# Kernel tuning notes

Hardware: AMD Instinct MI355X
Metric: run time of the kernel (lower is better)

The kernel has to match this reference:

```python
import jax, jax.numpy as jnp
import numpy as np

B, L, D_E = 2, 2048, 1024
H, D_Q = 16, 64
EPS = 1e-5


def setup_inputs() -> dict:
    key = jax.random.key(0)
    ks = jax.random.split(key, 12)
    s_in = 1.0 / np.sqrt(D_E)
    s_mid = 1.0 / np.sqrt(H * D_Q)
    return {
        "pre_q": jax.random.normal(ks[0], (B, L, D_E), jnp.float32),
        "pre_k": jax.random.normal(ks[1], (B, L, D_E), jnp.float32),
        "Wq": jax.random.normal(ks[2], (D_E, H * D_Q), jnp.float32) * s_in,
        "bq": jnp.zeros((H * D_Q,), jnp.float32),
        "Wk": jax.random.normal(ks[3], (D_E, H * D_Q), jnp.float32) * s_in,
        "bk": jnp.zeros((H * D_Q,), jnp.float32),
        "Wv": jax.random.normal(ks[4], (D_E, H * D_Q), jnp.float32) * s_in,
        "bv": jnp.zeros((H * D_Q,), jnp.float32),
        "Wo": jax.random.normal(ks[5], (H * D_Q, D_E), jnp.float32) * s_mid,
        "bo": jnp.zeros((D_E,), jnp.float32),
        "gamma": jnp.ones((D_E,), jnp.float32),
        "beta": jnp.zeros((D_E,), jnp.float32),
    }


def reference(pre_q, pre_k, Wq, bq, Wk, bk, Wv, bv, Wo, bo, gamma, beta):
    b, ql, _ = pre_q.shape
    kl = pre_k.shape[1]
    q = (pre_q @ Wq + bq).reshape(b, ql, H, D_Q)
    k = (pre_k @ Wk + bk).reshape(b, kl, H, D_Q)
    v = (pre_k @ Wv + bv).reshape(b, kl, H, D_Q)
    scores = jnp.einsum('bqhd,bkhd->bhqk', q, k) / jnp.sqrt(jnp.float32(D_Q))
    attn = jax.nn.softmax(scores, axis=-1)
    ctx = jnp.einsum('bhqk,bkhd->bqhd', attn, v).reshape(b, ql, H * D_Q)
    out = ctx @ Wo + bo
    x = pre_q + out
    mu = jnp.mean(x, axis=-1, keepdims=True)
    var = jnp.mean(jnp.square(x - mu), axis=-1, keepdims=True)
    return (x - mu) * jax.lax.rsqrt(var + EPS) * gamma + beta
```

## Files before the change

kernel.cpp:

```cpp
#include <hip/hip_runtime.h>
#include <hip/hip_bf16.h>
#include <cstdint>

typedef unsigned short ushort_t;
typedef __attribute__((ext_vector_type(8))) short short8;
typedef __attribute__((ext_vector_type(8))) __bf16 bf16x8;
typedef __attribute__((ext_vector_type(4))) float f32x4;
typedef __attribute__((ext_vector_type(4))) ushort_t ushort4v;
typedef __attribute__((ext_vector_type(2))) unsigned int uint2v;
typedef __attribute__((ext_vector_type(4))) unsigned int uint4v;

__device__ inline ushort_t f2bf(float f) {
    union { float f; unsigned u; } x; x.f = f;
    unsigned r = x.u + 0x7fffu + ((x.u >> 16) & 1u);
    return (ushort_t)(r >> 16);
}

__device__ inline unsigned pkbf(float a, float b) {
    __hip_bfloat162 h = __float22bfloat162_rn(float2{a, b});
    unsigned r;
    __builtin_memcpy(&r, &h, 4);
    return r;
}

__device__ inline unsigned pktrunc(float a, float b) {
    return __builtin_amdgcn_perm(__builtin_bit_cast(unsigned, b),
                                 __builtin_bit_cast(unsigned, a), 0x07060302u);
}

#if __has_builtin(__builtin_amdgcn_exp2f)
#define EXP2(x) __builtin_amdgcn_exp2f(x)
#else
#define EXP2(x) __builtin_exp2f(x)
#endif

__device__ inline bf16x8 ldfrag(const ushort_t* p) {
    short8 s = *(const short8*)p;
    return __builtin_bit_cast(bf16x8, s);
}

__device__ inline f32x4 mfma16(bf16x8 a, bf16x8 b, f32x4 c) {
    return __builtin_amdgcn_mfma_f32_16x16x32_bf16(a, b, c, 0, 0, 0);
}

__device__ inline void glds16(const ushort_t* g, ushort_t* l) {
    __builtin_amdgcn_global_load_lds((const __attribute__((address_space(1))) void*)g,
                                     (__attribute__((address_space(3))) void*)l, 16, 0, 0);
}

__global__ __launch_bounds__(256) void prep_k(const float* __restrict__ a, const float* __restrict__ b,
                                              ushort_t* __restrict__ oa, ushort_t* __restrict__ ob,
                                              const float* __restrict__ W0, const float* __restrict__ W1,
                                              const float* __restrict__ W2, const float* __restrict__ W3,
                                              ushort_t* __restrict__ wout) {
    const int blk = blockIdx.x;
    const int t = threadIdx.x;
    if (blk < 4096) {
        int i = (blk * 256 + t) * 4;
        float4 va = *(const float4*)(a + i);
        float4 vb = *(const float4*)(b + i);
        ushort4v pa = {f2bf(va.x), f2bf(va.y), f2bf(va.z), f2bf(va.w)};
        ushort4v pb = {f2bf(vb.x), f2bf(vb.y), f2bf(vb.z), f2bf(vb.w)};
        *(ushort4v*)(oa + i) = pa;
        *(ushort4v*)(ob + i) = pb;
    } else {
        const int rem = blk - 4096;
        const int z = rem >> 10;
        const int bx = (rem & 31) * 32, by = ((rem >> 5) & 31) * 32;
        const float* W = (z == 0) ? W0 : (z == 1) ? W1 : (z == 2) ? W2 : W3;
        ushort_t* o = wout + (size_t)z * (1u << 20);
        __shared__ float tile[32][33];
        const int tx = t & 31, ty = t >> 5;
#pragma unroll
        for (int r = 0; r < 4; ++r)
            tile[ty + r * 8][tx] = W[(size_t)(by + ty + r * 8) * 1024 + bx + tx];
        __syncthreads();
#pragma unroll
        for (int r = 0; r < 4; ++r)
            o[(size_t)(bx + ty + r * 8) * 1024 + by + tx] = f2bf(tile[tx][ty + r * 8]);
    }
}

template <int MODE>
__global__ __launch_bounds__(256) void gemm128(
    const ushort_t* __restrict__ A1, const ushort_t* __restrict__ A2,
    const ushort_t* __restrict__ Wt,
    const float* __restrict__ bias0, const float* __restrict__ bias1, const float* __restrict__ bias2,
    ushort_t* __restrict__ oQ, ushort_t* __restrict__ oK, ushort_t* __restrict__ oVt,
    const float* __restrict__ resid, float* __restrict__ oX) {
    const int t = threadIdx.x;
    const int phys = blockIdx.x;
    const int bid = (MODE == 0) ? (phys & 7) * 96 + (phys >> 3)
                                : (phys & 7) * 32 + (phys >> 3);
    int g, mb, nb;
    const float* bias;
    const ushort_t* Ab;
    const ushort_t* Wg;
    if (MODE == 0) {
        g = bid >> 8;
        const int rem = bid & 255;
        mb = rem >> 3;
        nb = rem & 7;
        Wg = Wt + (size_t)g * (1u << 20);
        bias = (g == 0) ? bias0 : (g == 1) ? bias1 : bias2;
        Ab = (g == 0) ? A1 : A2;
    } else {
        g = 0;
        mb = bid >> 3;
        nb = bid & 7;
        Wg = Wt;
        bias = bias0;
        Ab = A1;
    }
    const int m0 = mb * 128, n0 = nb * 128;

    __shared__ ushort_t As[3][128 * 32];
    __shared__ ushort_t Bs[3][128 * 32];
    const int row4 = t >> 2, c8 = (t & 3) * 8;
    const ushort_t* Ag = Ab + (size_t)(m0 + row4) * 1024 + c8;
    const ushort_t* Bg = Wg + (size_t)(n0 + row4) * 1024 + c8;
    const int ldst = row4 * 32 + c8;

    const int lane = t & 63, wid = t >> 6;
    const int wm = wid >> 1, wn = wid & 1;
    const int lr = lane & 15, lgp = lane >> 4, lk = lgp * 8;

    f32x4 acc[4][4];
#pragma unroll
    for (int j = 0; j < 4; ++j) {
        const f32x4 bj = *(const f32x4*)(bias + n0 + wn * 64 + j * 16 + 4 * lgp);
#pragma unroll
        for (int i = 0; i < 4; ++i) acc[j][i] = bj;
    }

#define STAGE(buf, kt)                                          \
    {                                                           \
        glds16(Ag + (kt), &As[buf][ldst]);                      \
        glds16(Ag + (kt) + 64 * 1024, &As[buf][ldst + 2048]);   \
        glds16(Bg + (kt), &Bs[buf][ldst]);                      \
        glds16(Bg + (kt) + 64 * 1024, &Bs[buf][ldst + 2048]);   \
    }

#define COMPUTE(buf)                                                              \
    {                                                                             \
        bf16x8 af[4], bfr[4];                                                     \
        _Pragma("unroll") for (int i = 0; i < 4; ++i)                             \
            af[i] = ldfrag(&As[buf][(wm * 64 + i * 16 + lr) * 32 + lk]);          \
        _Pragma("unroll") for (int j = 0; j < 4; ++j)                             \
            bfr[j] = ldfrag(&Bs[buf][(wn * 64 + j * 16 + lr) * 32 + lk]);         \
        __builtin_amdgcn_s_setprio(1);                                            \
        _Pragma("unroll") for (int j = 0; j < 4; ++j)                             \
            _Pragma("unroll") for (int i = 0; i < 4; ++i)                         \
                acc[j][i] = mfma16(bfr[j], af[i], acc[j][i]);                     \
        __builtin_amdgcn_s_setprio(0);                                            \
    }

#define GITER(it, buf, buf2)                                                      \
    {                                                                             \
        if ((it) <= 30) { asm volatile("s_waitcnt vmcnt(4)" ::: "memory"); }      \
        else            { asm volatile("s_waitcnt vmcnt(0)" ::: "memory"); }      \
        __syncthreads();                                                          \
        if ((it) + 2 < 32) STAGE(buf2, ((it) + 2) * 32);                          \
        COMPUTE(buf)                                                              \
    }

    STAGE(0, 0);
    STAGE(1, 32);
    for (int b3 = 0; b3 < 30; b3 += 3) {
        GITER(b3 + 0, 0, 2)
        GITER(b3 + 1, 1, 0)
        GITER(b3 + 2, 2, 1)
    }
    GITER(30, 0, 2)
    GITER(31, 1, 0)
#undef STAGE
#undef COMPUTE
#undef GITER

    const float qs = (MODE == 0 && g == 0) ? 0.18033688011f : 1.0f;

#pragma unroll
    for (int j = 0; j < 4; ++j) {
        const int n = n0 + wn * 64 + j * 16 + 4 * lgp;
#pragma unroll
        for (int i = 0; i < 4; ++i) {
            const f32x4 v = acc[j][i];
            const int m = m0 + wm * 64 + i * 16 + lr;
            if (MODE == 0) {
                const int b = m >> 11, ll = m & 2047;
                const int h = n >> 6, d = n & 63;
                if (g == 2) {
                    const int lp = (ll & ~63) | (ll & 32) | (((ll >> 2) & 3) << 3)
                                 | (((ll >> 4) & 1) << 2) | (ll & 3);
#pragma unroll
                    for (int jj = 0; jj < 4; ++jj)
                        oVt[((size_t)(b * 16 + h) * 64 + d + jj) * 2048 + lp] = f2bf(v[jj]);
                } else {
                    uint2v cw = {pkbf(v[0] * qs, v[1] * qs), pkbf(v[2] * qs, v[3] * qs)};
                    ushort_t* dst = (g == 0) ? oQ : oK;
                    *(uint2v*)(dst + (((size_t)(b * 16 + h) * 2048) + ll) * 64 + d) = cw;
                }
            } else {
                const float4 r = *(const float4*)(resid + (size_t)m * 1024 + n);
                float4 o;
                o.x = v[0] + r.x; o.y = v[1] + r.y; o.z = v[2] + r.z; o.w = v[3] + r.w;
                *(float4*)(oX + (size_t)m * 1024 + n) = o;
            }
        }
    }
}

__global__ __launch_bounds__(256, 2) void attn_k(const ushort_t* __restrict__ Qg, const ushort_t* __restrict__ Kg,
                                                 const ushort_t* __restrict__ Vtg, ushort_t* __restrict__ Cg) {
    __shared__ ushort_t Ks[2][8 * 512];
    __shared__ ushort_t Vs[2][8 * 512];

    const int t = threadIdx.x;
    const int lane = t & 63, w = t >> 6;
    const int bid = blockIdx.x;
    const int xcd = bid & 7, j = bid >> 3;
    const int bh = (xcd << 2) | (j >> 4);
    const int qb = j & 15;
    const int q0 = qb * 128 + w * 32;
    const int lr = lane & 15, g = lane >> 4;
    const int srow = lane & 15, sch = lane >> 4;

    const ushort_t* Kbase = Kg + (size_t)bh * (2048 * 64);
    const ushort_t* Vbase = Vtg + (size_t)bh * (64 * 2048);

    const ushort_t* QpA = Qg + ((size_t)bh * 2048 + q0 + lr) * 64 + g * 8;
    const bf16x8 qA0 = ldfrag(QpA), qA1 = ldfrag(QpA + 32);
    const bf16x8 qB0 = ldfrag(QpA + 16 * 64), qB1 = ldfrag(QpA + 16 * 64 + 32);

    f32x4 oA[4] = {}, oB[4] = {};
    float lA = 0.f, lB = 0.f;

#define STAGE(buf, kt)                                                                        \
    {                                                                                         \
        glds16(Kbase + (size_t)((kt) + 16 * w + srow) * 64 + sch * 8, &Ks[buf][w * 512 + lane * 8]);            \
        glds16(Kbase + (size_t)((kt) + 16 * w + srow) * 64 + 32 + sch * 8, &Ks[buf][(4 + w) * 512 + lane * 8]); \
        glds16(Vbase + (size_t)(16 * w + srow) * 2048 + (kt) + sch * 8, &Vs[buf][(2 * w) * 512 + lane * 8]);    \
        glds16(Vbase + (size_t)(16 * w + srow) * 2048 + (kt) + 32 + sch * 8, &Vs[buf][(2 * w + 1) * 512 + lane * 8]); \
    }

#define COMPUTE(BUF)                                                                      \
    {                                                                                     \
        f32x4 stA[4], stB[4];                                                             \
        _Pragma("unroll") for (int f = 0; f < 4; ++f) {                                   \
            const bf16x8 k0 = ldfrag(&Ks[BUF][f * 512 + lane * 8]);                       \
            const bf16x8 k1 = ldfrag(&Ks[BUF][(4 + f) * 512 + lane * 8]);                 \
            f32x4 sA = {}, sB = {};                                                       \
            sA = mfma16(k0, qA0, sA);                                                     \
            sA = mfma16(k1, qA1, sA);                                                     \
            sB = mfma16(k0, qB0, sB);                                                     \
            sB = mfma16(k1, qB1, sB);                                                     \
            stA[f] = sA;                                                                  \
            stB[f] = sB;                                                                  \
        }                                                                                 \
        unsigned pkA[8], pkB[8];                                                          \
        float rsA = 0.f, rsB = 0.f;                                                       \
        _Pragma("unroll") for (int f = 0; f < 4; ++f) {                                   \
            const float a0 = EXP2(stA[f][0]);                                             \
            const float a1 = EXP2(stA[f][1]);                                             \
            const float a2 = EXP2(stA[f][2]);                                             \
            const float a3 = EXP2(stA[f][3]);                                             \
            rsA += (a0 + a1) + (a2 + a3);                                                 \
            pkA[2 * f] = pktrunc(a0, a1);                                                 \
            pkA[2 * f + 1] = pktrunc(a2, a3);                                             \
            const float b0 = EXP2(stB[f][0]);                                             \
            const float b1 = EXP2(stB[f][1]);                                             \
            const float b2 = EXP2(stB[f][2]);                                             \
            const float b3 = EXP2(stB[f][3]);                                             \
            rsB += (b0 + b1) + (b2 + b3);                                                 \
            pkB[2 * f] = pktrunc(b0, b1);                                                 \
            pkB[2 * f + 1] = pktrunc(b2, b3);                                             \
        }                                                                                 \
        lA += rsA;                                                                        \
        lB += rsB;                                                                        \
        _Pragma("unroll") for (int b = 0; b < 2; ++b) {                                   \
            const uint4v ua = {pkA[4 * b], pkA[4 * b + 1], pkA[4 * b + 2], pkA[4 * b + 3]}; \
            const uint4v ub = {pkB[4 * b], pkB[4 * b + 1], pkB[4 * b + 2], pkB[4 * b + 3]}; \
            const bf16x8 pA = __builtin_bit_cast(bf16x8, ua);                             \
            const bf16x8 pB = __builtin_bit_cast(bf16x8, ub);                             \
            _Pragma("unroll") for (int df = 0; df < 4; ++df) {                            \
                const bf16x8 vf = ldfrag(&Vs[BUF][(2 * df + b) * 512 + (g * 16 + lr) * 8]); \
                oA[df] = mfma16(vf, pA, oA[df]);                                          \
                oB[df] = mfma16(vf, pB, oB[df]);                                          \
            }                                                                             \
        }                                                                                 \
    }

    STAGE(0, 0);
    asm volatile("s_waitcnt vmcnt(0)" ::: "memory");
    __syncthreads();

    for (int kt2 = 0; kt2 < 2048; kt2 += 128) {
        STAGE(1, kt2 + 64);
        COMPUTE(0)
        asm volatile("s_waitcnt vmcnt(0)" ::: "memory");
        __syncthreads();
        if (kt2 + 128 < 2048) STAGE(0, kt2 + 128);
        COMPUTE(1)
        asm volatile("s_waitcnt vmcnt(0)" ::: "memory");
        __syncthreads();
    }
#undef STAGE
#undef COMPUTE

    lA += __shfl_xor(lA, 16, 64);
    lA += __shfl_xor(lA, 32, 64);
    lB += __shfl_xor(lB, 16, 64);
    lB += __shfl_xor(lB, 32, 64);

    const int bb = bh >> 4, hh = bh & 15;
    {
        const float inv = 1.0f / lA;
        ushort_t* cp = Cg + ((size_t)(bb * 2048 + q0 + lr) * 1024) + hh * 64;
#pragma unroll
        for (int df = 0; df < 4; ++df) {
            uint2v cw = {pkbf(oA[df][0] * inv, oA[df][1] * inv), pkbf(oA[df][2] * inv, oA[df][3] * inv)};
            *(uint2v*)(cp + 16 * df + 4 * g) = cw;
        }
    }
    {
        const float inv = 1.0f / lB;
        ushort_t* cp = Cg + ((size_t)(bb * 2048 + q0 + 16 + lr) * 1024) + hh * 64;
#pragma unroll
        for (int df = 0; df < 4; ++df) {
            uint2v cw = {pkbf(oB[df][0] * inv, oB[df][1] * inv), pkbf(oB[df][2] * inv, oB[df][3] * inv)};
            *(uint2v*)(cp + 16 * df + 4 * g) = cw;
        }
    }
}

__global__ __launch_bounds__(256) void ln_k(const float* __restrict__ X, const float* __restrict__ gamma,
                                            const float* __restrict__ beta, float* __restrict__ out) {
    const int row = blockIdx.x, t = threadIdx.x;
    const float4 x = ((const float4*)(X + (size_t)row * 1024))[t];
    float s = x.x + x.y + x.z + x.w;
    float s2 = x.x * x.x + x.y * x.y + x.z * x.z + x.w * x.w;
#pragma unroll
    for (int m = 1; m < 64; m <<= 1) {
        s += __shfl_xor(s, m, 64);
        s2 += __shfl_xor(s2, m, 64);
    }
    __shared__ float rs[4], rq[4];
    if ((t & 63) == 0) { rs[t >> 6] = s; rq[t >> 6] = s2; }
    __syncthreads();
    const float S = rs[0] + rs[1] + rs[2] + rs[3];
    const float S2 = rq[0] + rq[1] + rq[2] + rq[3];
    const float mu = S * (1.0f / 1024.0f);
    const float var = S2 * (1.0f / 1024.0f) - mu * mu;
    const float r = rsqrtf(var + 1e-5f);
    const float4 gg = ((const float4*)gamma)[t];
    const float4 bb = ((const float4*)beta)[t];
    float4 o;
    o.x = (x.x - mu) * r * gg.x + bb.x;
    o.y = (x.y - mu) * r * gg.y + bb.y;
    o.z = (x.z - mu) * r * gg.z + bb.z;
    o.w = (x.w - mu) * r * gg.w + bb.w;
    ((float4*)(out + (size_t)row * 1024))[t] = o;
}

extern "C" void kernel_launch(void* const* d_in, const int* in_sizes, int n_in,
                              void* d_out, int out_size, void* d_ws, size_t ws_size,
                              hipStream_t stream) {
    (void)in_sizes; (void)n_in; (void)out_size; (void)ws_size;
    const float* pre_q = (const float*)d_in[0];
    const float* pre_k = (const float*)d_in[1];
    const float* Wq = (const float*)d_in[2];
    const float* bq = (const float*)d_in[3];
    const float* Wk = (const float*)d_in[4];
    const float* bk = (const float*)d_in[5];
    const float* Wv = (const float*)d_in[6];
    const float* bv = (const float*)d_in[7];
    const float* Wo = (const float*)d_in[8];
    const float* bo = (const float*)d_in[9];
    const float* gamma = (const float*)d_in[10];
    const float* beta = (const float*)d_in[11];
    float* out = (float*)d_out;
    char* ws = (char*)d_ws;
    const size_t MB = 1024 * 1024;
    ushort_t* Xq = (ushort_t*)(ws);
    ushort_t* Xk = (ushort_t*)(ws + 8 * MB);
    ushort_t* Wt = (ushort_t*)(ws + 16 * MB);
    ushort_t* Qb = (ushort_t*)(ws + 24 * MB);
    ushort_t* Kb = (ushort_t*)(ws + 32 * MB);
    ushort_t* Vt = (ushort_t*)(ws + 40 * MB);
    ushort_t* CTX = (ushort_t*)(ws + 48 * MB);
    float* Xres = (float*)(ws + 24 * MB);

    prep_k<<<8192, 256, 0, stream>>>(pre_q, pre_k, Xq, Xk, Wq, Wk, Wv, Wo, Wt);
    gemm128<0><<<768, 256, 0, stream>>>(Xq, Xk, Wt, bq, bk, bv, Qb, Kb, Vt, nullptr, nullptr);
    attn_k<<<512, 256, 0, stream>>>(Qb, Kb, Vt, CTX);
    gemm128<1><<<256, 256, 0, stream>>>(CTX, nullptr, Wt + 3 * (1u << 20), bo, nullptr, nullptr,
                                        nullptr, nullptr, nullptr, pre_q, Xres);
    ln_k<<<4096, 256, 0, stream>>>(Xres, gamma, beta, out);
}
```

Measured before the change: 125.6 us.

## Fuse fp32-to-bf16 activation conversion into QKV GEMM and store residual as bf16

After: 124.4 us (median of 2 runs). Within noise of the previous version (-0.9%).

```diff
diff --git a/kernel.cpp b/kernel.cpp
--- a/kernel.cpp
+++ b/kernel.cpp
@@ -23,6 +23,11 @@
     return r;
 }
 
+__device__ inline float bf2f(ushort_t u) {
+    unsigned v = (unsigned)u << 16;
+    return __builtin_bit_cast(float, v);
+}
+
 __device__ inline unsigned pktrunc(float a, float b) {
     return __builtin_amdgcn_perm(__builtin_bit_cast(unsigned, b),
                                  __builtin_bit_cast(unsigned, a), 0x07060302u);
@@ -48,53 +53,40 @@
                                      (__attribute__((address_space(3))) void*)l, 16, 0, 0);
 }
 
-__global__ __launch_bounds__(256) void prep_k(const float* __restrict__ a, const float* __restrict__ b,
-                                              ushort_t* __restrict__ oa, ushort_t* __restrict__ ob,
-                                              const float* __restrict__ W0, const float* __restrict__ W1,
+__global__ __launch_bounds__(256) void prep_k(const float* __restrict__ W0, const float* __restrict__ W1,
                                               const float* __restrict__ W2, const float* __restrict__ W3,
                                               ushort_t* __restrict__ wout) {
     const int blk = blockIdx.x;
     const int t = threadIdx.x;
-    if (blk < 4096) {
-        int i = (blk * 256 + t) * 4;
-        float4 va = *(const float4*)(a + i);
-        float4 vb = *(const float4*)(b + i);
-        ushort4v pa = {f2bf(va.x), f2bf(va.y), f2bf(va.z), f2bf(va.w)};
-        ushort4v pb = {f2bf(vb.x), f2bf(vb.y), f2bf(vb.z), f2bf(vb.w)};
-        *(ushort4v*)(oa + i) = pa;
-        *(ushort4v*)(ob + i) = pb;
-    } else {
-        const int rem = blk - 4096;
-        const int z = rem >> 10;
-        const int bx = (rem & 31) * 32, by = ((rem >> 5) & 31) * 32;
-        const float* W = (z == 0) ? W0 : (z == 1) ? W1 : (z == 2) ? W2 : W3;
-        ushort_t* o = wout + (size_t)z * (1u << 20);
-        __shared__ float tile[32][33];
-        const int tx = t & 31, ty = t >> 5;
-#pragma unroll
-        for (int r = 0; r < 4; ++r)
-            tile[ty + r * 8][tx] = W[(size_t)(by + ty + r * 8) * 1024 + bx + tx];
-        __syncthreads();
-#pragma unroll
-        for (int r = 0; r < 4; ++r)
-            o[(size_t)(bx + ty + r * 8) * 1024 + by + tx] = f2bf(tile[tx][ty + r * 8]);
-    }
+    const int z = blk >> 10;
+    const int bx = (blk & 31) * 32, by = ((blk >> 5) & 31) * 32;
+    const float* W = (z == 0) ? W0 : (z == 1) ? W1 : (z == 2) ? W2 : W3;
+    ushort_t* o = wout + (size_t)z * (1u << 20);
+    __shared__ float tile[32][33];
+    const int tx = t & 31, ty = t >> 5;
+#pragma unroll
+    for (int r = 0; r < 4; ++r)
+        tile[ty + r * 8][tx] = W[(size_t)(by + ty + r * 8) * 1024 + bx + tx];
+    __syncthreads();
+#pragma unroll
+    for (int r = 0; r < 4; ++r)
+        o[(size_t)(bx + ty + r * 8) * 1024 + by + tx] = f2bf(tile[tx][ty + r * 8]);
 }
 
 template <int MODE>
 __global__ __launch_bounds__(256) void gemm128(
-    const ushort_t* __restrict__ A1, const ushort_t* __restrict__ A2,
+    const float* __restrict__ Af1, const float* __restrict__ Af2,
+    const ushort_t* __restrict__ A1,
     const ushort_t* __restrict__ Wt,
     const float* __restrict__ bias0, const float* __restrict__ bias1, const float* __restrict__ bias2,
     ushort_t* __restrict__ oQ, ushort_t* __restrict__ oK, ushort_t* __restrict__ oVt,
-    const float* __restrict__ resid, float* __restrict__ oX) {
+    const float* __restrict__ resid, ushort_t* __restrict__ oXb) {
     const int t = threadIdx.x;
     const int phys = blockIdx.x;
     const int bid = (MODE == 0) ? (phys & 7) * 96 + (phys >> 3)
                                 : (phys & 7) * 32 + (phys >> 3);
     int g, mb, nb;
     const float* bias;
-    const ushort_t* Ab;
     const ushort_t* Wg;
     if (MODE == 0) {
         g = bid >> 8;
@@ -103,23 +95,27 @@
         nb = rem & 7;
         Wg = Wt + (size_t)g * (1u << 20);
         bias = (g == 0) ? bias0 : (g == 1) ? bias1 : bias2;
-        Ab = (g == 0) ? A1 : A2;
     } else {
         g = 0;
         mb = bid >> 3;
         nb = bid & 7;
         Wg = Wt;
         bias = bias0;
-        Ab = A1;
     }
     const int m0 = mb * 128, n0 = nb * 128;
 
     __shared__ ushort_t As[3][128 * 32];
     __shared__ ushort_t Bs[3][128 * 32];
     const int row4 = t >> 2, c8 = (t & 3) * 8;
-    const ushort_t* Ag = Ab + (size_t)(m0 + row4) * 1024 + c8;
     const ushort_t* Bg = Wg + (size_t)(n0 + row4) * 1024 + c8;
     const int ldst = row4 * 32 + c8;
+
+    const float* Agf = nullptr;
+    const ushort_t* Ag = nullptr;
+    if (MODE == 0)
+        Agf = ((g == 0) ? Af1 : Af2) + (size_t)(m0 + row4) * 1024 + c8;
+    else
+        Ag = A1 + (size_t)(m0 + row4) * 1024 + c8;
 
     const int lane = t & 63, wid = t >> 6;
     const int wm = wid >> 1, wn = wid & 1;
@@ -133,12 +129,36 @@
         for (int i = 0; i < 4; ++i) acc[j][i] = bj;
     }
 
-#define STAGE(buf, kt)                                          \
+    f32x4 a0, a1, a2, a3;
+
+#define A_LOAD(kt)                                              \
+    {                                                           \
+        a0 = *(const f32x4*)(Agf + (kt));                       \
+        a1 = *(const f32x4*)(Agf + (kt) + 4);                   \
+        a2 = *(const f32x4*)(Agf + (kt) + 64 * 1024);           \
+        a3 = *(const f32x4*)(Agf + (kt) + 64 * 1024 + 4);       \
+    }
+
+#define A_WRITE(buf)                                                               \
+    {                                                                              \
+        uint4v w0 = {pkbf(a0[0], a0[1]), pkbf(a0[2], a0[3]),                       \
+                     pkbf(a1[0], a1[1]), pkbf(a1[2], a1[3])};                      \
+        *(uint4v*)&As[buf][ldst] = w0;                                             \
+        uint4v w1 = {pkbf(a2[0], a2[1]), pkbf(a2[2], a2[3]),                       \
+                     pkbf(a3[0], a3[1]), pkbf(a3[2], a3[3])};                      \
+        *(uint4v*)&As[buf][ldst + 2048] = w1;                                      \
+    }
+
+#define B_STAGE(buf, kt)                                        \
+    {                                                           \
+        glds16(Bg + (kt), &Bs[buf][ldst]);                      \
+        glds16(Bg + (kt) + 64 * 1024, &Bs[buf][ldst + 2048]);   \
+    }
+
+#define A_STAGE_G(buf, kt)                                      \
     {                                                           \
         glds16(Ag + (kt), &As[buf][ldst]);                      \
         glds16(Ag + (kt) + 64 * 1024, &As[buf][ldst + 2048]);   \
-        glds16(Bg + (kt), &Bs[buf][ldst]);                      \
-        glds16(Bg + (kt) + 64 * 1024, &Bs[buf][ldst + 2048]);   \
     }
 
 #define COMPUTE(buf)                                                              \
@@ -155,27 +175,55 @@
         __builtin_amdgcn_s_setprio(0);                                            \
     }
 
-#define GITER(it, buf, buf2)                                                      \
+#define GITER0(it, buf, buf2)                                                     \
+    {                                                                             \
+        if ((it) <= 30) { asm volatile("s_waitcnt vmcnt(2)" ::: "memory"); }      \
+        else            { asm volatile("s_waitcnt vmcnt(0)" ::: "memory"); }      \
+        A_WRITE(buf)                                                              \
+        __syncthreads();                                                          \
+        if ((it) + 1 < 32) A_LOAD(((it) + 1) * 32)                                \
+        if ((it) + 2 < 32) B_STAGE(buf2, ((it) + 2) * 32)                         \
+        COMPUTE(buf)                                                              \
+    }
+
+#define GITER1(it, buf, buf2)                                                     \
     {                                                                             \
         if ((it) <= 30) { asm volatile("s_waitcnt vmcnt(4)" ::: "memory"); }      \
         else            { asm volatile("s_waitcnt vmcnt(0)" ::: "memory"); }      \
         __syncthreads();                                                          \
-        if ((it) + 2 < 32) STAGE(buf2, ((it) + 2) * 32);                          \
+        if ((it) + 2 < 32) { A_STAGE_G(buf2, ((it) + 2) * 32) B_STAGE(buf2, ((it) + 2) * 32) } \
         COMPUTE(buf)                                                              \
     }
 
-    STAGE(0, 0);
-    STAGE(1, 32);
-    for (int b3 = 0; b3 < 30; b3 += 3) {
-        GITER(b3 + 0, 0, 2)
-        GITER(b3 + 1, 1, 0)
-        GITER(b3 + 2, 2, 1)
-    }
-    GITER(30, 0, 2)
-    GITER(31, 1, 0)
-#undef STAGE
+    if (MODE == 0) {
+        B_STAGE(0, 0);
+        A_LOAD(0);
+        B_STAGE(1, 32);
+        for (int b3 = 0; b3 < 30; b3 += 3) {
+            GITER0(b3 + 0, 0, 2)
+            GITER0(b3 + 1, 1, 0)
+            GITER0(b3 + 2, 2, 1)
+        }
+        GITER0(30, 0, 2)
+        GITER0(31, 1, 0)
+    } else {
+        A_STAGE_G(0, 0) B_STAGE(0, 0);
+        A_STAGE_G(1, 32) B_STAGE(1, 32);
+        for (int b3 = 0; b3 < 30; b3 += 3) {
+            GITER1(b3 + 0, 0, 2)
+            GITER1(b3 + 1, 1, 0)
+            GITER1(b3 + 2, 2, 1)
+        }
+        GITER1(30, 0, 2)
+        GITER1(31, 1, 0)
+    }
+#undef A_LOAD
+#undef A_WRITE
+#undef B_STAGE
+#undef A_STAGE_G
 #undef COMPUTE
-#undef GITER
+#undef GITER0
+#undef GITER1
 
     const float qs = (MODE == 0 && g == 0) ? 0.18033688011f : 1.0f;
 
@@ -202,9 +250,8 @@
                 }
             } else {
                 const float4 r = *(const float4*)(resid + (size_t)m * 1024 + n);
-                float4 o;
-                o.x = v[0] + r.x; o.y = v[1] + r.y; o.z = v[2] + r.z; o.w = v[3] + r.w;
-                *(float4*)(oX + (size_t)m * 1024 + n) = o;
+                uint2v cw = {pkbf(v[0] + r.x, v[1] + r.y), pkbf(v[2] + r.z, v[3] + r.w)};
+                *(uint2v*)(oXb + (size_t)m * 1024 + n) = cw;
             }
         }
     }
@@ -333,12 +380,13 @@
     }
 }
 
-__global__ __launch_bounds__(256) void ln_k(const float* __restrict__ X, const float* __restrict__ gamma,
+__global__ __launch_bounds__(256) void ln_k(const ushort_t* __restrict__ X, const float* __restrict__ gamma,
                                             const float* __restrict__ beta, float* __restrict__ out) {
     const int row = blockIdx.x, t = threadIdx.x;
-    const float4 x = ((const float4*)(X + (size_t)row * 1024))[t];
-    float s = x.x + x.y + x.z + x.w;
-    float s2 = x.x * x.x + x.y * x.y + x.z * x.z + x.w * x.w;
+    const ushort4v xr = ((const ushort4v*)(X + (size_t)row * 1024))[t];
+    const float x0 = bf2f(xr[0]), x1 = bf2f(xr[1]), x2 = bf2f(xr[2]), x3 = bf2f(xr[3]);
+    float s = (x0 + x1) + (x2 + x3);
+    float s2 = (x0 * x0 + x1 * x1) + (x2 * x2 + x3 * x3);
 #pragma unroll
     for (int m = 1; m < 64; m <<= 1) {
         s += __shfl_xor(s, m, 64);
@@ -355,10 +403,10 @@
     const float4 gg = ((const float4*)gamma)[t];
     const float4 bb = ((const float4*)beta)[t];
     float4 o;
-    o.x = (x.x - mu) * r * gg.x + bb.x;
-    o.y = (x.y - mu) * r * gg.y + bb.y;
-    o.z = (x.z - mu) * r * gg.z + bb.z;
-    o.w = (x.w - mu) * r * gg.w + bb.w;
+    o.x = (x0 - mu) * r * gg.x + bb.x;
+    o.y = (x1 - mu) * r * gg.y + bb.y;
+    o.z = (x2 - mu) * r * gg.z + bb.z;
+    o.w = (x3 - mu) * r * gg.w + bb.w;
     ((float4*)(out + (size_t)row * 1024))[t] = o;
 }
 
@@ -381,19 +429,18 @@
     float* out = (float*)d_out;
     char* ws = (char*)d_ws;
     const size_t MB = 1024 * 1024;
-    ushort_t* Xq = (ushort_t*)(ws);
-    ushort_t* Xk = (ushort_t*)(ws + 8 * MB);
     ushort_t* Wt = (ushort_t*)(ws + 16 * MB);
     ushort_t* Qb = (ushort_t*)(ws + 24 * MB);
     ushort_t* Kb = (ushort_t*)(ws + 32 * MB);
     ushort_t* Vt = (ushort_t*)(ws + 40 * MB);
     ushort_t* CTX = (ushort_t*)(ws + 48 * MB);
-    float* Xres = (float*)(ws + 24 * MB);
-
-    prep_k<<<8192, 256, 0, stream>>>(pre_q, pre_k, Xq, Xk, Wq, Wk, Wv, Wo, Wt);
-    gemm128<0><<<768, 256, 0, stream>>>(Xq, Xk, Wt, bq, bk, bv, Qb, Kb, Vt, nullptr, nullptr);
+    ushort_t* Xres = (ushort_t*)(ws);
+
+    prep_k<<<4096, 256, 0, stream>>>(Wq, Wk, Wv, Wo, Wt);
+    gemm128<0><<<768, 256, 0, stream>>>(pre_q, pre_k, nullptr, Wt, bq, bk, bv,
+                                        Qb, Kb, Vt, nullptr, nullptr);
     attn_k<<<512, 256, 0, stream>>>(Qb, Kb, Vt, CTX);
-    gemm128<1><<<256, 256, 0, stream>>>(CTX, nullptr, Wt + 3 * (1u << 20), bo, nullptr, nullptr,
+    gemm128<1><<<256, 256, 0, stream>>>(nullptr, nullptr, CTX, Wt + 3 * (1u << 20), bo, nullptr, nullptr,
                                         nullptr, nullptr, nullptr, pre_q, Xres);
     ln_k<<<4096, 256, 0, stream>>>(Xres, gamma, beta, out);
 }
```
